# Kernel optimization log

Hardware: AMD Instinct MI355X
Metric: run time of the kernel (lower is better)

The kernel has to match this reference:

```python
import jax, jax.numpy as jnp
import numpy as np
import math

N_HEAD = 12
BLOCK = 256  # local attention block size (ls)
EPS = 1e-6


def _rotate(x):
    # pairs (a, b) -> (-b, a) over last dim (matches rotate_embeddings)
    a = x[..., 0::2]
    b = x[..., 1::2]
    return jnp.stack([-b, a], axis=-1).reshape(x.shape)


def setup_inputs() -> dict:
    key = jax.random.key(0)
    k1, k2, k3 = jax.random.split(key, 3)
    B, T, C = 4, 8192, 768
    s = 0.02
    return {
        "x": jax.random.normal(k1, (B, T, C), jnp.float32),
        "w_qkv": jax.random.normal(k2, (C, 3 * C), jnp.float32) * s,
        "w_ln": jnp.ones((C,), jnp.float32),
        "w_proj": jax.random.normal(k3, (C, C), jnp.float32) * s,
    }


def reference(x, w_qkv, w_ln, w_proj):
    B, T, C = x.shape
    nh, ls = N_HEAD, BLOCK
    hd = C // nh
    ng = T // ls

    xb = x.reshape(B, ng, ls, C)
    qkv = xb @ w_qkv                                   # (B,ng,ls,3C)
    q, k, v = jnp.split(qkv, 3, axis=-1)

    # QK RMSNorm over full embedding dim (before head split)
    def rms(t):
        return t * jax.lax.rsqrt(jnp.mean(t * t, axis=-1, keepdims=True) + EPS) * w_ln
    q, k = rms(q), rms(k)

    # split heads: (B,ng,nh,ls,hd)
    def heads(t):
        return jnp.swapaxes(t.reshape(B, ng, ls, nh, hd), 2, 3)
    q, k, v = heads(q), heads(k), heads(v)

    # RoPE (repo layout: freqs tiled via cat((ts,ts)), interleaved pair rotation)
    pos = 10000.0 ** ((-2.0 * jnp.arange(0, hd, 2, dtype=jnp.float32) - 1.0) / hd)
    ts = jnp.arange(ls, dtype=jnp.float32)[:, None] * pos[None, :]   # (ls, hd/2)
    rot = jnp.concatenate([ts, ts], axis=-1)                          # (ls, hd)
    cos, sin = jnp.cos(rot), jnp.sin(rot)
    q = q * cos + _rotate(q) * sin
    k = k * cos + _rotate(k) * sin

    # block-causal scores: causal only within each local block
    scale = 1.0 / math.sqrt(hd)
    att = jnp.einsum('bgnqd,bgnkd->bgnqk', q, k) * scale              # (B,ng,nh,ls,ls)
    mask = jnp.tril(jnp.ones((ls, ls), dtype=bool))
    att = jnp.where(mask, att, -jnp.finfo(att.dtype).max)
    att = jax.nn.softmax(att, axis=-1)
    y = jnp.einsum('bgnqk,bgnkd->bgnqd', att, v)                      # (B,ng,nh,ls,hd)

    y = jnp.swapaxes(y, 2, 3).reshape(B, ng, ls, C)
    y = y @ w_proj
    return y.reshape(B, T, C)
```

## Files before the change

### kernel.cpp

```cpp
#include <hip/hip_runtime.h>
#include <math.h>

typedef __attribute__((ext_vector_type(8))) short bf16x8;
typedef __attribute__((ext_vector_type(4))) short bf16x4;
typedef __attribute__((ext_vector_type(2))) short bf16x2;
typedef __attribute__((ext_vector_type(4))) float f32x4;

#define NH 12
#define HD 64
#define C0 768
#define C3 2304
#define LS 256

static __device__ __forceinline__ float bf2f(short u) {
  union { unsigned int i; float f; } c;
  c.i = ((unsigned int)(unsigned short)u) << 16;
  return c.f;
}
static __device__ __forceinline__ short f2bf(float f) {
  union { float f; unsigned int i; } c; c.f = f;
  unsigned int x = c.i;
  x += 0x7fffu + ((x >> 16) & 1u);
  return (short)(x >> 16);
}
static __device__ __forceinline__ unsigned pk2(float a, float b) {
  return (unsigned)(unsigned short)f2bf(a) | ((unsigned)(unsigned short)f2bf(b) << 16);
}

static __device__ __forceinline__ void gload_lds16(const short* g, const short* l) {
  unsigned long long ga = (unsigned long long)g;
  unsigned int la = (unsigned int)(unsigned long long)l;
  __builtin_amdgcn_global_load_lds(
      (const __attribute__((address_space(1))) void*)ga,
      (__attribute__((address_space(3))) void*)la, 16, 0, 0);
}

__global__ __launch_bounds__(256) void cast_kernel(const float* __restrict__ in,
                                                   short* __restrict__ out, int nquads) {
  int i = blockIdx.x * blockDim.x + threadIdx.x;
  int stride = gridDim.x * blockDim.x;
  for (; i < nquads; i += stride) {
    float4 v = ((const float4*)in)[i];
    bf16x4 o = { f2bf(v.x), f2bf(v.y), f2bf(v.z), f2bf(v.w) };
    ((bf16x4*)out)[i] = o;
  }
}

__global__ __launch_bounds__(256) void cast_transpose_kernel(const float* __restrict__ in,
                                                             short* __restrict__ out,
                                                             int K, int N) {
  __shared__ float tile[32][33];
  int n0 = blockIdx.x * 32, k0 = blockIdx.y * 32;
  int tx = threadIdx.x & 31, ty = threadIdx.x >> 5;
#pragma unroll
  for (int i = 0; i < 32; i += 8)
    tile[ty + i][tx] = in[(long)(k0 + ty + i) * N + n0 + tx];
  __syncthreads();
#pragma unroll
  for (int i = 0; i < 32; i += 8)
    out[(long)(n0 + ty + i) * K + k0 + tx] = f2bf(tile[tx][ty + i]);
}

__global__ void rope_tab_kernel(float* __restrict__ cost, float* __restrict__ sint) {
  int t = blockIdx.x, d = threadIdx.x;
  int i = d & 31;
  float freq = powf(10000.0f, -(float)(4 * i + 1) / 64.0f);
  float th = (float)t * freq;
  cost[t * 64 + d] = cosf(th);
  sint[t * 64 + d] = sinf(th);
}

#define PH_PRE                                         \
  __builtin_amdgcn_s_barrier();                        \
  __builtin_amdgcn_s_setprio(1);
#define PH_POST                                        \
  __builtin_amdgcn_s_setprio(0);                       \
  asm volatile("s_waitcnt lgkmcnt(0)" ::: "memory");   \
  __builtin_amdgcn_s_barrier();
#define PH_POSTV                                       \
  __builtin_amdgcn_s_setprio(0);                       \
  asm volatile("s_waitcnt lgkmcnt(0)" ::: "memory");   \
  asm volatile("s_waitcnt vmcnt(4)" ::: "memory");     \
  __builtin_amdgcn_s_barrier();
#define MMQ(MH, NP)                                                                \
  { _Pragma("unroll") for (int f_ = 0; f_ < 4; ++f_)                               \
      _Pragma("unroll") for (int n_ = 0; n_ < 2; ++n_)                             \
        _Pragma("unroll") for (int k_ = 0; k_ < 2; ++k_)                           \
          acc[(MH)*4 + f_][(NP)*2 + n_] = __builtin_amdgcn_mfma_f32_16x16x32_bf16( \
              af[f_*2 + k_], bfv[((NP)*2 + n_)*2 + k_],                            \
              acc[(MH)*4 + f_][(NP)*2 + n_], 0, 0, 0); }

template <int OUT_F32>
__global__ __launch_bounds__(512, 2) void gemm8p_kernel(const short* __restrict__ A,
                                                        const short* __restrict__ Bt,
                                                        void* __restrict__ Cout,
                                                        int N, int K, int nbn) {
  __shared__ short lds[65536];
  int t = threadIdx.x, lane = t & 63, wave = t >> 6;
  int lr = lane & 15, lg = lane >> 4;
  int wm = (wave >> 2) * 128, wn = (wave & 3) * 64;
  int id = blockIdx.x;
  int cpx = gridDim.x >> 3;
  int sw = (id & 7) * cpx + (id >> 3);
  int bm = sw / nbn, bn = sw % nbn;
  const short* Abase = A + (long)bm * 256 * K;
  const short* Bbase = Bt + (long)bn * 256 * K;
  int srow = t >> 3;
  int scol = ((t & 7) ^ (srow & 7)) * 8;
  int smax = K >> 4;

  f32x4 acc[8][4];
#pragma unroll
  for (int m = 0; m < 8; ++m)
#pragma unroll
    for (int n = 0; n < 4; ++n) acc[m][n] = (f32x4){0.f, 0.f, 0.f, 0.f};

  bf16x8 af[8], bfv[8];

  auto STAGE = [&](int s) {
    int slot = s & 3;
    int Tg = (s < smax) ? (s >> 2) : 0;
    const short* base = (slot & 2) ? Abase : Bbase;
    const short* g = base + (long)((slot & 1) * 128 + srow) * K + Tg * 64 + scol;
    int lb = ((s >> 2) & 1) * 32768 + ((slot >> 1) ^ 1) * 16384 + (slot & 1) * 8192 + t * 8;
    gload_lds16(g, &lds[lb]);
    gload_lds16(g + (long)64 * K, &lds[lb + 4096]);
  };
  auto LDA = [&](int b, int mh) {
#pragma unroll
    for (int f = 0; f < 4; ++f) {
      int R = wm + mh * 64 + f * 16 + lr;
      int rb = b * 32768 + R * 64;
      int s8 = R & 7;
      af[f * 2 + 0] = *(bf16x8*)&lds[rb + ((lg ^ s8) << 3)];
      af[f * 2 + 1] = *(bf16x8*)&lds[rb + (((4 + lg) ^ s8) << 3)];
    }
  };
  auto LDB = [&](int b, int nh) {
#pragma unroll
    for (int j = 0; j < 2; ++j) {
      int R = wn + (nh * 2 + j) * 16 + lr;
      int rb = b * 32768 + 16384 + R * 64;
      int s8 = R & 7;
      bfv[(nh * 2 + j) * 2 + 0] = *(bf16x8*)&lds[rb + ((lg ^ s8) << 3)];
      bfv[(nh * 2 + j) * 2 + 1] = *(bf16x8*)&lds[rb + (((4 + lg) ^ s8) << 3)];
    }
  };

  STAGE(0); STAGE(1); STAGE(2); STAGE(3); STAGE(4); STAGE(5);
  asm volatile("s_waitcnt vmcnt(4)" ::: "memory");
  __builtin_amdgcn_s_barrier();

  int iters = K >> 7;
  for (int i = 0; i < iters; ++i) {
    int si = 8 * i + 6;
    LDA(0, 0); LDB(0, 0);
    STAGE(si + 0);
    PH_PRE; MMQ(0, 0); PH_POST;
    LDB(0, 1);
    STAGE(si + 1);
    PH_PRE; MMQ(0, 1); PH_POST;
    LDA(0, 1);
    STAGE(si + 2);
    PH_PRE; MMQ(1, 0); PH_POST;
    STAGE(si + 3);
    PH_PRE; MMQ(1, 1); PH_POSTV;
    LDA(1, 0); LDB(1, 0);
    STAGE(si + 4);
    PH_PRE; MMQ(0, 0); PH_POST;
    LDB(1, 1);
    STAGE(si + 5);
    PH_PRE; MMQ(0, 1); PH_POST;
    LDA(1, 1);
    STAGE(si + 6);
    PH_PRE; MMQ(1, 0); PH_POST;
    STAGE(si + 7);
    PH_PRE; MMQ(1, 1); PH_POSTV;
  }

  long crow0 = (long)bm * 256 + wm;
  long ccol0 = (long)bn * 256 + wn;
#pragma unroll
  for (int f = 0; f < 8; ++f)
#pragma unroll
    for (int n = 0; n < 4; ++n)
#pragma unroll
      for (int r = 0; r < 4; ++r) {
        long row = crow0 + (f >> 2) * 64 + (f & 3) * 16 + lg * 4 + r;
        long col = ccol0 + n * 16 + lr;
        float v = acc[f][n][r];
        if (OUT_F32) ((float*)Cout)[row * N + col] = v;
        else ((short*)Cout)[row * N + col] = f2bf(v);
      }
}

__global__ __launch_bounds__(384) void norm_rope_kernel(short* __restrict__ QKV,
    const float* __restrict__ w_ln, const float* __restrict__ cost,
    const float* __restrict__ sint) {
  int row = blockIdx.x;
  int t = row & 255;
  int i = threadIdx.x;
  bool isq = i < 192;
  int e0 = (i - (isq ? 0 : 192)) * 4;
  long off = (long)row * C3 + (isq ? 0 : C0) + e0;
  bf16x4 v4 = *(const bf16x4*)&QKV[off];
  float a = bf2f(v4.x), b = bf2f(v4.y), c = bf2f(v4.z), d = bf2f(v4.w);
  float ss = a * a + b * b + c * c + d * d;
#pragma unroll
  for (int o = 32; o > 0; o >>= 1) ss += __shfl_down(ss, o);
  __shared__ float red[6];
  if ((i & 63) == 0) red[i >> 6] = ss;
  __syncthreads();
  float s3 = isq ? (red[0] + red[1] + red[2]) : (red[3] + red[4] + red[5]);
  float r = rsqrtf(s3 * (1.0f / 768.0f) + 1e-6f);
  float4 wl = *(const float4*)&w_ln[e0];
  int d0 = e0 & 63;
  float4 cs = *(const float4*)&cost[t * 64 + d0];
  float4 sn = *(const float4*)&sint[t * 64 + d0];
  float n0 = a * r * wl.x, n1 = b * r * wl.y, n2 = c * r * wl.z, n3 = d * r * wl.w;
  bf16x4 o;
  o.x = f2bf(n0 * cs.x - n1 * sn.x);
  o.y = f2bf(n1 * cs.y + n0 * sn.y);
  o.z = f2bf(n2 * cs.z - n3 * sn.z);
  o.w = f2bf(n3 * cs.w + n2 * sn.w);
  *(bf16x4*)&QKV[off] = o;
}

__global__ __launch_bounds__(512, 3) void attn_kernel(const short* __restrict__ QKV,
                                                      short* __restrict__ Y) {
  __shared__ short Ks[256 * 64];
  __shared__ short Vt[64 * 256];
  int blk = blockIdx.x;
  int bg = blk / NH, h = blk % NH;
  const long base = (long)bg * LS * C3 + h * HD;
  int tid = threadIdx.x, lane = tid & 63, wave = tid >> 6;
  int lr = lane & 15, lg = lane >> 4;

#pragma unroll
  for (int it = 0; it < 4; ++it) {
    int q = it * 512 + tid;
    int row = q >> 3, cp = q & 7;
    int gcp = cp ^ (row & 7);
    gload_lds16(QKV + base + (long)row * C3 + C0 + gcp * 8, &Ks[q * 8]);
  }
#pragma unroll
  for (int it = 0; it < 8; ++it) {
    int e = tid * 4 + it * 2048;
    int k = e >> 6, n = e & 63;
    bf16x4 v = *(const bf16x4*)&QKV[base + (long)k * C3 + 2 * C0 + n];
#pragma unroll
    for (int j = 0; j < 4; ++j) {
      int nn = n + j;
      Vt[nn * 256 + (((k >> 3) ^ (nn & 7)) << 3) + (k & 7)] = v[j];
    }
  }
  asm volatile("s_waitcnt vmcnt(0)" ::: "memory");
  __syncthreads();

  int addrA = (((lane >> 4) & 1) * 32 + lr) * 4;
  int addrB = addrA + 64;
  bool selhi = (lane & 32) != 0;

  for (int tt = 0; tt < 2; ++tt) {
    int tile = (tt == 0) ? wave : (15 - wave);
    int m0 = tile * 16;
    bf16x8 qf[2];
#pragma unroll
    for (int ks = 0; ks < 2; ++ks)
      qf[ks] = *(const bf16x8*)&QKV[base + (long)(m0 + lr) * C3 + ks * 32 + lg * 8];

    f32x4 zero4 = {0.f, 0.f, 0.f, 0.f};
    f32x4 accs[16];
#pragma unroll
    for (int n = 0; n < 16; ++n) accs[n] = zero4;

    __builtin_amdgcn_s_setprio(1);
#pragma unroll
    for (int n = 0; n < 16; ++n) {
      if (n <= tile) {
        int row = n * 16 + lr, sw = row & 7;
        bf16x8 k0 = *(bf16x8*)&Ks[row * 64 + ((lg ^ sw) << 3)];
        bf16x8 k1 = *(bf16x8*)&Ks[row * 64 + (((4 + lg) ^ sw) << 3)];
        accs[n] = __builtin_amdgcn_mfma_f32_16x16x32_bf16(k0, qf[0], accs[n], 0, 0, 0);
        accs[n] = __builtin_amdgcn_mfma_f32_16x16x32_bf16(k1, qf[1], accs[n], 0, 0, 0);
      }
    }
    __builtin_amdgcn_s_setprio(0);

    float tm[16];
#pragma unroll
    for (int n = 0; n < 16; ++n) {
      if (n <= tile) {
        if (n == tile) {
#pragma unroll
          for (int r = 0; r < 4; ++r)
            accs[n][r] = (lg * 4 + r <= lr) ? accs[n][r] : -1e30f;
        }
        float m01 = fmaxf(accs[n][0], accs[n][1]);
        float m23 = fmaxf(accs[n][2], accs[n][3]);
        tm[n] = fmaxf(m01, m23);
      } else {
        tm[n] = -1e30f;
      }
    }
#pragma unroll
    for (int st = 1; st < 16; st <<= 1)
#pragma unroll
      for (int j = 0; j < 16; j += 2 * st) tm[j] = fmaxf(tm[j], tm[j + st]);
    float mloc = tm[0];
    mloc = fmaxf(mloc, __shfl_xor(mloc, 16));
    mloc = fmaxf(mloc, __shfl_xor(mloc, 32));

    float ts[16];
#pragma unroll
    for (int n = 0; n < 16; ++n) {
      if (n <= tile) {
#pragma unroll
        for (int r = 0; r < 4; ++r) accs[n][r] = __expf((accs[n][r] - mloc) * 0.125f);
        float s01 = accs[n][0] + accs[n][1];
        float s23 = accs[n][2] + accs[n][3];
        ts[n] = s01 + s23;
      } else {
        ts[n] = 0.f;
      }
    }
#pragma unroll
    for (int st = 1; st < 16; st <<= 1)
#pragma unroll
      for (int j = 0; j < 16; j += 2 * st) ts[j] += ts[j + st];
    float s = ts[0];
    s += __shfl_xor(s, 16);
    s += __shfl_xor(s, 32);
    float rs = 1.0f / s;
    float rv[4];
#pragma unroll
    for (int r = 0; r < 4; ++r) {
      union { float f; int i; } c; c.f = rs;
      union { int i; float f; } o;
      o.i = __builtin_amdgcn_ds_bpermute((lg * 4 + r) * 4, c.i);
      rv[r] = o.f;
    }

    int ktmax = (m0 + 15) >> 5;
    f32x4 yacc[4];
#pragma unroll
    for (int n2 = 0; n2 < 4; ++n2) yacc[n2] = zero4;
#pragma unroll
    for (int kt = 0; kt < 8; ++kt) {
      if (kt <= ktmax) {
        int n0 = 2 * kt, n1 = 2 * kt + 1;
        unsigned a01_0 = pk2(accs[n0][0], accs[n0][1]);
        unsigned a23_0 = pk2(accs[n0][2], accs[n0][3]);
        unsigned a01_1 = (n1 <= tile) ? pk2(accs[n1][0], accs[n1][1]) : 0u;
        unsigned a23_1 = (n1 <= tile) ? pk2(accs[n1][2], accs[n1][3]) : 0u;
        union { unsigned u[4]; bf16x8 v; } af;
        unsigned g0a = (unsigned)__builtin_amdgcn_ds_bpermute(addrA, (int)a01_0);
        unsigned g0b = (unsigned)__builtin_amdgcn_ds_bpermute(addrA, (int)a01_1);
        unsigned g1a = (unsigned)__builtin_amdgcn_ds_bpermute(addrA, (int)a23_0);
        unsigned g1b = (unsigned)__builtin_amdgcn_ds_bpermute(addrA, (int)a23_1);
        unsigned g2a = (unsigned)__builtin_amdgcn_ds_bpermute(addrB, (int)a01_0);
        unsigned g2b = (unsigned)__builtin_amdgcn_ds_bpermute(addrB, (int)a01_1);
        unsigned g3a = (unsigned)__builtin_amdgcn_ds_bpermute(addrB, (int)a23_0);
        unsigned g3b = (unsigned)__builtin_amdgcn_ds_bpermute(addrB, (int)a23_1);
        af.u[0] = selhi ? g0b : g0a;
        af.u[1] = selhi ? g1b : g1a;
        af.u[2] = selhi ? g2b : g2a;
        af.u[3] = selhi ? g3b : g3a;
        int ac = kt * 32 + lg * 8;
        __builtin_amdgcn_s_setprio(1);
#pragma unroll
        for (int n2 = 0; n2 < 4; ++n2) {
          int vn = n2 * 16 + lr;
          bf16x8 vb = *(bf16x8*)&Vt[vn * 256 + (((ac >> 3) ^ (vn & 7)) << 3)];
          yacc[n2] = __builtin_amdgcn_mfma_f32_16x16x32_bf16(af.v, vb, yacc[n2], 0, 0, 0);
        }
        __builtin_amdgcn_s_setprio(0);
      }
    }

#pragma unroll
    for (int n2 = 0; n2 < 4; ++n2) {
#pragma unroll
      for (int r = 0; r < 4; ++r) {
        int row = m0 + lg * 4 + r, d = n2 * 16 + lr;
        Y[((long)(bg * LS + row)) * C0 + h * HD + d] = f2bf(yacc[n2][r] * rv[r]);
      }
    }
  }
}

extern "C" void kernel_launch(void* const* d_in, const int* in_sizes, int n_in,
                              void* d_out, int out_size, void* d_ws, size_t ws_size,
                              hipStream_t stream) {
  (void)in_sizes; (void)n_in; (void)out_size; (void)ws_size;
  const float* x = (const float*)d_in[0];
  const float* w_qkv = (const float*)d_in[1];
  const float* w_ln = (const float*)d_in[2];
  const float* w_proj = (const float*)d_in[3];
  float* out = (float*)d_out;

  char* ws = (char*)d_ws;
  short* Xb      = (short*)(ws + 0);
  short* QKV     = (short*)(ws + 50331648);
  short* Yb      = (short*)(ws + 201326592);
  short* WqkvT   = (short*)(ws + 251658240);
  short* WprojT  = (short*)(ws + 255197184);
  float* cost    = (float*)(ws + 256376832);
  float* sint    = (float*)(ws + 256442368);

  cast_kernel<<<2048, 256, 0, stream>>>(x, Xb, (4 * 8192 * C0) / 4);
  cast_transpose_kernel<<<dim3(C3 / 32, C0 / 32), 256, 0, stream>>>(w_qkv, WqkvT, C0, C3);
  cast_transpose_kernel<<<dim3(C0 / 32, C0 / 32), 256, 0, stream>>>(w_proj, WprojT, C0, C0);
  rope_tab_kernel<<<256, 64, 0, stream>>>(cost, sint);

  gemm8p_kernel<0><<<(C3 / 256) * (32768 / 256), 512, 0, stream>>>(Xb, WqkvT, QKV,
                                                                   C3, C0, C3 / 256);
  norm_rope_kernel<<<32768, 384, 0, stream>>>(QKV, w_ln, cost, sint);
  attn_kernel<<<128 * NH, 512, 0, stream>>>(QKV, Yb);
  gemm8p_kernel<1><<<(C0 / 256) * (32768 / 256), 512, 0, stream>>>(Yb, WprojT, out,
                                                                   C0, C0, C0 / 256);
}
```

Before: 326.8 us.

## Switch GEMMs to 32x32x16 MFMA with fragment-packed operands and a reworked pipeline

The cast kernels now write the inputs and weights into a pre-packed MFMA fragment layout, so the GEMM can load LDS fragments with simple contiguous lane reads. Both GEMMs move from 16x16x32 to 32x32x16 bf16 MFMA. The software pipeline is rescheduled so LDS reads and global-to-LDS stages run after the MFMA phase and are waited on with a vmcnt wait before each barrier. The projection GEMM keeps row-major A with XOR swizzle. The aim is fewer LDS instructions and better MFMA throughput, at the cost of a more complex packing step and correctness risk in the fragment mapping.

```diff
diff --git a/kernel.cpp b/kernel.cpp
--- a/kernel.cpp
+++ b/kernel.cpp
@@ -5,12 +5,14 @@
 typedef __attribute__((ext_vector_type(4))) short bf16x4;
 typedef __attribute__((ext_vector_type(2))) short bf16x2;
 typedef __attribute__((ext_vector_type(4))) float f32x4;
+typedef __attribute__((ext_vector_type(16))) float f32x16;
 
 #define NH 12
 #define HD 64
 #define C0 768
 #define C3 2304
 #define LS 256
+#define KT12 12
 
 static __device__ __forceinline__ float bf2f(short u) {
   union { unsigned int i; float f; } c;
@@ -35,30 +37,61 @@
       (__attribute__((address_space(3))) void*)la, 16, 0, 0);
 }
 
-__global__ __launch_bounds__(256) void cast_kernel(const float* __restrict__ in,
-                                                   short* __restrict__ out, int nquads) {
-  int i = blockIdx.x * blockDim.x + threadIdx.x;
-  int stride = gridDim.x * blockDim.x;
-  for (; i < nquads; i += stride) {
-    float4 v = ((const float4*)in)[i];
-    bf16x4 o = { f2bf(v.x), f2bf(v.y), f2bf(v.z), f2bf(v.w) };
-    ((bf16x4*)out)[i] = o;
-  }
-}
-
-__global__ __launch_bounds__(256) void cast_transpose_kernel(const float* __restrict__ in,
-                                                             short* __restrict__ out,
-                                                             int K, int N) {
-  __shared__ float tile[32][33];
-  int n0 = blockIdx.x * 32, k0 = blockIdx.y * 32;
-  int tx = threadIdx.x & 31, ty = threadIdx.x >> 5;
-#pragma unroll
-  for (int i = 0; i < 32; i += 8)
-    tile[ty + i][tx] = in[(long)(k0 + ty + i) * N + n0 + tx];
+__global__ __launch_bounds__(256) void cast_pack_A_kernel(const float* __restrict__ x,
+                                                          short* __restrict__ Apk) {
+  __shared__ short sb[256 * 64];
+  int bm = blockIdx.x, kt = blockIdx.y, t = threadIdx.x;
+#pragma unroll
+  for (int i = 0; i < 8; ++i) {
+    int seg = i * 256 + t;
+    int row = seg >> 3, sc = (seg & 7) * 8;
+    const float* src = x + ((long)(bm * 256 + row)) * C0 + kt * 64 + sc;
+    float4 v0 = *(const float4*)src;
+    float4 v1 = *(const float4*)(src + 4);
+    short* d = &sb[row * 64 + sc];
+    d[0] = f2bf(v0.x); d[1] = f2bf(v0.y); d[2] = f2bf(v0.z); d[3] = f2bf(v0.w);
+    d[4] = f2bf(v1.x); d[5] = f2bf(v1.y); d[6] = f2bf(v1.z); d[7] = f2bf(v1.w);
+  }
   __syncthreads();
 #pragma unroll
-  for (int i = 0; i < 32; i += 8)
-    out[(long)(n0 + ty + i) * K + k0 + tx] = f2bf(tile[tx][ty + i]);
+  for (int i = 0; i < 8; ++i) {
+    int c = i * 256 + t;
+    int l = c & 63, f = c >> 6;
+    int ks = f & 3, mt = (f >> 2) & 3, mh = f >> 4;
+    int row = mh * 128 + mt * 32 + (l & 31);
+    int kk = ks * 16 + (l >> 5) * 8;
+    bf16x8 v = *(bf16x8*)&sb[row * 64 + kk];
+    *(bf16x8*)&Apk[(((long)bm * KT12 + kt) * 2048 + c) * 8] = v;
+  }
+}
+
+__global__ __launch_bounds__(256) void cast_pack_B_kernel(const float* __restrict__ w,
+                                                          short* __restrict__ Bpk, int N) {
+  __shared__ short sb[256 * 64];
+  int bn = blockIdx.x, kt = blockIdx.y, t = threadIdx.x;
+#pragma unroll
+  for (int i = 0; i < 8; ++i) {
+    int seg = i * 256 + t;
+    int k = seg >> 5, nc = (seg & 31) * 8;
+    const float* src = w + ((long)(kt * 64 + k)) * N + bn * 256 + nc;
+    float4 v0 = *(const float4*)src;
+    float4 v1 = *(const float4*)(src + 4);
+    sb[(nc + 0) * 64 + k] = f2bf(v0.x); sb[(nc + 1) * 64 + k] = f2bf(v0.y);
+    sb[(nc + 2) * 64 + k] = f2bf(v0.z); sb[(nc + 3) * 64 + k] = f2bf(v0.w);
+    sb[(nc + 4) * 64 + k] = f2bf(v1.x); sb[(nc + 5) * 64 + k] = f2bf(v1.y);
+    sb[(nc + 6) * 64 + k] = f2bf(v1.z); sb[(nc + 7) * 64 + k] = f2bf(v1.w);
+  }
+  __syncthreads();
+#pragma unroll
+  for (int i = 0; i < 8; ++i) {
+    int c = i * 256 + t;
+    int l = c & 63, f = c >> 6;
+    int ks = f & 3, nt = (f >> 2) & 1, wng = f >> 3;
+    int col = wng * 64 + nt * 32 + (l & 31);
+    int kk = ks * 16 + (l >> 5) * 8;
+    bf16x8 v = *(bf16x8*)&sb[col * 64 + kk];
+    *(bf16x8*)&Bpk[(((long)bn * KT12 + kt) * 2048 + c) * 8] = v;
+  }
 }
 
 __global__ void rope_tab_kernel(float* __restrict__ cost, float* __restrict__ sint) {
@@ -70,125 +103,136 @@
   sint[t * 64 + d] = sinf(th);
 }
 
-#define PH_PRE                                         \
+#define PH_OPEN                                        \
   __builtin_amdgcn_s_barrier();                        \
+  asm volatile("s_waitcnt lgkmcnt(0)" ::: "memory");   \
+  __builtin_amdgcn_sched_barrier(0);                   \
   __builtin_amdgcn_s_setprio(1);
-#define PH_POST                                        \
-  __builtin_amdgcn_s_setprio(0);                       \
-  asm volatile("s_waitcnt lgkmcnt(0)" ::: "memory");   \
+#define PH_MID __builtin_amdgcn_s_setprio(0);
+#define PH_CLOSE                                       \
+  asm volatile("s_waitcnt vmcnt(2)" ::: "memory");     \
   __builtin_amdgcn_s_barrier();
-#define PH_POSTV                                       \
-  __builtin_amdgcn_s_setprio(0);                       \
-  asm volatile("s_waitcnt lgkmcnt(0)" ::: "memory");   \
-  asm volatile("s_waitcnt vmcnt(4)" ::: "memory");     \
-  __builtin_amdgcn_s_barrier();
-#define MMQ(MH, NP)                                                                \
-  { _Pragma("unroll") for (int f_ = 0; f_ < 4; ++f_)                               \
-      _Pragma("unroll") for (int n_ = 0; n_ < 2; ++n_)                             \
-        _Pragma("unroll") for (int k_ = 0; k_ < 2; ++k_)                           \
-          acc[(MH)*4 + f_][(NP)*2 + n_] = __builtin_amdgcn_mfma_f32_16x16x32_bf16( \
-              af[f_*2 + k_], bfv[((NP)*2 + n_)*2 + k_],                            \
-              acc[(MH)*4 + f_][(NP)*2 + n_], 0, 0, 0); }
-
-template <int OUT_F32>
-__global__ __launch_bounds__(512, 2) void gemm8p_kernel(const short* __restrict__ A,
-                                                        const short* __restrict__ Bt,
+#define MM8(ASET, BSET, MP, NT)                                                     \
+  { _Pragma("unroll") for (int m2_ = 0; m2_ < 2; ++m2_)                             \
+      _Pragma("unroll") for (int ks_ = 0; ks_ < 4; ++ks_)                           \
+        acc[(MP)*2 + m2_][NT] = __builtin_amdgcn_mfma_f32_32x32x16_bf16(            \
+            ASET[m2_ * 4 + ks_], BSET[ks_], acc[(MP)*2 + m2_][NT], 0, 0, 0); }
+
+template <int OUT_F32, int PACKED_A>
+__global__ __launch_bounds__(512, 2) void gemm32_kernel(const short* __restrict__ Apk,
+                                                        const short* __restrict__ Bpk,
+                                                        const short* __restrict__ Arm,
                                                         void* __restrict__ Cout,
                                                         int N, int K, int nbn) {
   __shared__ short lds[65536];
   int t = threadIdx.x, lane = t & 63, wave = t >> 6;
-  int lr = lane & 15, lg = lane >> 4;
-  int wm = (wave >> 2) * 128, wn = (wave & 3) * 64;
+  int wm = (wave >> 2) * 128, wng = wave & 3, wn = wng * 64, mh = wave >> 2;
   int id = blockIdx.x;
   int cpx = gridDim.x >> 3;
   int sw = (id & 7) * cpx + (id >> 3);
   int bm = sw / nbn, bn = sw % nbn;
-  const short* Abase = A + (long)bm * 256 * K;
-  const short* Bbase = Bt + (long)bn * 256 * K;
-  int srow = t >> 3;
-  int scol = ((t & 7) ^ (srow & 7)) * 8;
-  int smax = K >> 4;
-
-  f32x4 acc[8][4];
-#pragma unroll
-  for (int m = 0; m < 8; ++m)
-#pragma unroll
-    for (int n = 0; n < 4; ++n) acc[m][n] = (f32x4){0.f, 0.f, 0.f, 0.f};
-
-  bf16x8 af[8], bfv[8];
+
+  f32x16 acc[4][2];
+#pragma unroll
+  for (int m = 0; m < 4; ++m)
+#pragma unroll
+    for (int n = 0; n < 2; ++n)
+#pragma unroll
+      for (int r = 0; r < 16; ++r) acc[m][n][r] = 0.f;
+
+  bf16x8 a0[8], a1[8], b0[4], b1[4];
 
   auto STAGE = [&](int s) {
-    int slot = s & 3;
-    int Tg = (s < smax) ? (s >> 2) : 0;
-    const short* base = (slot & 2) ? Abase : Bbase;
-    const short* g = base + (long)((slot & 1) * 128 + srow) * K + Tg * 64 + scol;
-    int lb = ((s >> 2) & 1) * 32768 + ((slot >> 1) ^ 1) * 16384 + (slot & 1) * 8192 + t * 8;
-    gload_lds16(g, &lds[lb]);
-    gload_lds16(g + (long)64 * K, &lds[lb + 4096]);
+    if (s >= 4 * KT12) return;
+    int q = s & 3, Ts = s >> 2;
+    int bb = (Ts & 1) * 32768;
+    if (q < 2) {
+      if (PACKED_A) {
+        int c = q * 1024 + t;
+        const short* src = Apk + ((long)bm * KT12 + Ts) * 16384 + (long)c * 8;
+        gload_lds16(src, &lds[bb + c * 8]);
+        gload_lds16(src + 4096, &lds[bb + (c + 512) * 8]);
+      } else {
+        int row = q * 128 + (t >> 3);
+        int cr = q * 1024 + t;
+        const short* s1 = Arm + ((long)(bm * 256 + row)) * K + Ts * 64 + ((t & 7) ^ (row & 7)) * 8;
+        gload_lds16(s1, &lds[bb + cr * 8]);
+        int row2 = row + 64;
+        const short* s2 = Arm + ((long)(bm * 256 + row2)) * K + Ts * 64 + ((t & 7) ^ (row2 & 7)) * 8;
+        gload_lds16(s2, &lds[bb + (cr + 512) * 8]);
+      }
+    } else {
+      int c = (q - 2) * 1024 + t;
+      const short* src = Bpk + ((long)bn * KT12 + Ts) * 16384 + (long)c * 8;
+      gload_lds16(src, &lds[bb + 16384 + c * 8]);
+      gload_lds16(src + 4096, &lds[bb + 16384 + (c + 512) * 8]);
+    }
   };
-  auto LDA = [&](int b, int mh) {
-#pragma unroll
-    for (int f = 0; f < 4; ++f) {
-      int R = wm + mh * 64 + f * 16 + lr;
-      int rb = b * 32768 + R * 64;
-      int s8 = R & 7;
-      af[f * 2 + 0] = *(bf16x8*)&lds[rb + ((lg ^ s8) << 3)];
-      af[f * 2 + 1] = *(bf16x8*)&lds[rb + (((4 + lg) ^ s8) << 3)];
+  auto LDA = [&](bf16x8* d, int b, int mhalf) {
+    if (PACKED_A) {
+#pragma unroll
+      for (int m2 = 0; m2 < 2; ++m2)
+#pragma unroll
+        for (int ks = 0; ks < 4; ++ks)
+          d[m2 * 4 + ks] =
+              *(bf16x8*)&lds[b * 32768 + ((mh * 16 + (mhalf * 2 + m2) * 4 + ks) * 64 + lane) * 8];
+    } else {
+#pragma unroll
+      for (int m2 = 0; m2 < 2; ++m2)
+#pragma unroll
+        for (int ks = 0; ks < 4; ++ks) {
+          int row = wm + (mhalf * 2 + m2) * 32 + (lane & 31);
+          int g = (ks * 2 + (lane >> 5)) ^ (row & 7);
+          d[m2 * 4 + ks] = *(bf16x8*)&lds[b * 32768 + row * 64 + g * 8];
+        }
     }
   };
-  auto LDB = [&](int b, int nh) {
-#pragma unroll
-    for (int j = 0; j < 2; ++j) {
-      int R = wn + (nh * 2 + j) * 16 + lr;
-      int rb = b * 32768 + 16384 + R * 64;
-      int s8 = R & 7;
-      bfv[(nh * 2 + j) * 2 + 0] = *(bf16x8*)&lds[rb + ((lg ^ s8) << 3)];
-      bfv[(nh * 2 + j) * 2 + 1] = *(bf16x8*)&lds[rb + (((4 + lg) ^ s8) << 3)];
-    }
+  auto LDB = [&](bf16x8* d, int b, int nt) {
+#pragma unroll
+    for (int ks = 0; ks < 4; ++ks)
+      d[ks] = *(bf16x8*)&lds[b * 32768 + 16384 + ((wng * 8 + nt * 4 + ks) * 64 + lane) * 8];
   };
 
-  STAGE(0); STAGE(1); STAGE(2); STAGE(3); STAGE(4); STAGE(5);
-  asm volatile("s_waitcnt vmcnt(4)" ::: "memory");
+  for (int s = 0; s < 7; ++s) STAGE(s);
+  asm volatile("s_waitcnt vmcnt(6)" ::: "memory");
   __builtin_amdgcn_s_barrier();
-
-  int iters = K >> 7;
-  for (int i = 0; i < iters; ++i) {
-    int si = 8 * i + 6;
-    LDA(0, 0); LDB(0, 0);
-    STAGE(si + 0);
-    PH_PRE; MMQ(0, 0); PH_POST;
-    LDB(0, 1);
-    STAGE(si + 1);
-    PH_PRE; MMQ(0, 1); PH_POST;
-    LDA(0, 1);
-    STAGE(si + 2);
-    PH_PRE; MMQ(1, 0); PH_POST;
-    STAGE(si + 3);
-    PH_PRE; MMQ(1, 1); PH_POSTV;
-    LDA(1, 0); LDB(1, 0);
-    STAGE(si + 4);
-    PH_PRE; MMQ(0, 0); PH_POST;
-    LDB(1, 1);
-    STAGE(si + 5);
-    PH_PRE; MMQ(0, 1); PH_POST;
-    LDA(1, 1);
-    STAGE(si + 6);
-    PH_PRE; MMQ(1, 0); PH_POST;
-    STAGE(si + 7);
-    PH_PRE; MMQ(1, 1); PH_POSTV;
+  LDA(a0, 0, 0);
+  LDB(b0, 0, 0);
+  LDB(b1, 0, 1);
+
+  for (int it = 0; it < KT12 / 2; ++it) {
+    int P0 = 8 * it;
+    PH_OPEN; MM8(a0, b0, 0, 0); PH_MID;
+    LDA(a1, 0, 1); STAGE(P0 + 7); PH_CLOSE;
+    PH_OPEN; MM8(a0, b1, 0, 1); PH_MID;
+    LDA(a0, 1, 0); STAGE(P0 + 8); PH_CLOSE;
+    PH_OPEN; MM8(a1, b0, 1, 0); PH_MID;
+    LDB(b0, 1, 0); STAGE(P0 + 9); PH_CLOSE;
+    PH_OPEN; MM8(a1, b1, 1, 1); PH_MID;
+    LDB(b1, 1, 1); STAGE(P0 + 10); PH_CLOSE;
+    PH_OPEN; MM8(a0, b0, 0, 0); PH_MID;
+    LDA(a1, 1, 1); STAGE(P0 + 11); PH_CLOSE;
+    PH_OPEN; MM8(a0, b1, 0, 1); PH_MID;
+    LDA(a0, 0, 0); STAGE(P0 + 12); PH_CLOSE;
+    PH_OPEN; MM8(a1, b0, 1, 0); PH_MID;
+    LDB(b0, 0, 0); STAGE(P0 + 13); PH_CLOSE;
+    PH_OPEN; MM8(a1, b1, 1, 1); PH_MID;
+    LDB(b1, 0, 1); STAGE(P0 + 14); PH_CLOSE;
   }
 
   long crow0 = (long)bm * 256 + wm;
   long ccol0 = (long)bn * 256 + wn;
-#pragma unroll
-  for (int f = 0; f < 8; ++f)
-#pragma unroll
-    for (int n = 0; n < 4; ++n)
-#pragma unroll
-      for (int r = 0; r < 4; ++r) {
-        long row = crow0 + (f >> 2) * 64 + (f & 3) * 16 + lg * 4 + r;
-        long col = ccol0 + n * 16 + lr;
-        float v = acc[f][n][r];
+  int rbase = 4 * (lane >> 5);
+  int cl = lane & 31;
+#pragma unroll
+  for (int mt = 0; mt < 4; ++mt)
+#pragma unroll
+    for (int nt = 0; nt < 2; ++nt)
+#pragma unroll
+      for (int reg = 0; reg < 16; ++reg) {
+        long row = crow0 + mt * 32 + (reg & 3) + 8 * (reg >> 2) + rbase;
+        long col = ccol0 + nt * 32 + cl;
+        float v = acc[mt][nt][reg];
         if (OUT_F32) ((float*)Cout)[row * N + col] = v;
         else ((short*)Cout)[row * N + col] = f2bf(v);
       }
@@ -400,23 +444,23 @@
   float* out = (float*)d_out;
 
   char* ws = (char*)d_ws;
-  short* Xb      = (short*)(ws + 0);
+  short* Apk     = (short*)(ws + 0);
   short* QKV     = (short*)(ws + 50331648);
   short* Yb      = (short*)(ws + 201326592);
-  short* WqkvT   = (short*)(ws + 251658240);
-  short* WprojT  = (short*)(ws + 255197184);
+  short* WqkvPk  = (short*)(ws + 251658240);
+  short* WprojPk = (short*)(ws + 255197184);
   float* cost    = (float*)(ws + 256376832);
   float* sint    = (float*)(ws + 256442368);
 
-  cast_kernel<<<2048, 256, 0, stream>>>(x, Xb, (4 * 8192 * C0) / 4);
-  cast_transpose_kernel<<<dim3(C3 / 32, C0 / 32), 256, 0, stream>>>(w_qkv, WqkvT, C0, C3);
-  cast_transpose_kernel<<<dim3(C0 / 32, C0 / 32), 256, 0, stream>>>(w_proj, WprojT, C0, C0);
+  cast_pack_A_kernel<<<dim3(128, KT12), 256, 0, stream>>>(x, Apk);
+  cast_pack_B_kernel<<<dim3(9, KT12), 256, 0, stream>>>(w_qkv, WqkvPk, C3);
+  cast_pack_B_kernel<<<dim3(3, KT12), 256, 0, stream>>>(w_proj, WprojPk, C0);
   rope_tab_kernel<<<256, 64, 0, stream>>>(cost, sint);
 
-  gemm8p_kernel<0><<<(C3 / 256) * (32768 / 256), 512, 0, stream>>>(Xb, WqkvT, QKV,
-                                                                   C3, C0, C3 / 256);
+  gemm32_kernel<0, 1><<<128 * 9, 512, 0, stream>>>(Apk, WqkvPk, nullptr, QKV,
+                                                   C3, C0, 9);
   norm_rope_kernel<<<32768, 384, 0, stream>>>(QKV, w_ln, cost, sint);
   attn_kernel<<<128 * NH, 512, 0, stream>>>(QKV, Yb);
-  gemm8p_kernel<1><<<(C0 / 256) * (32768 / 256), 512, 0, stream>>>(Yb, WprojT, out,
-                                                                   C0, C0, C0 / 256);
-}
+  gemm32_kernel<1, 0><<<128 * 3, 512, 0, stream>>>(nullptr, WprojPk, Yb, out,
+                                                   C0, C0, 3);
+}
```

New measurement: 373.0 us. 1.14x slower.

## Use 128x128 prepacked-B GEMM for projection and wave-per-row norm/rope

Applied to the files above, without the earlier changes.

Replaces the 256x256-tile GEMM for the output projection with a new 128x128-tile kernel that uses 32x32x16 MFMAs and a pre-packed B operand laid out in fragment order, so it can be loaded with contiguous direct-to-LDS loads. The smaller tile raises the block count from 384 to 1536 for better CU occupancy on the N=768 GEMM. The norm/rope kernel is also restructured to one wave per q or k row, with shuffle-only reduction and wider loads, which removes the LDS reduction and the block barrier. A new cast-and-pack kernel prepares w_proj in that layout. The trade-offs are less data reuse per tile and a simpler double-buffered pipeline with a full wait on every K step.

```diff
diff --git a/kernel.cpp b/kernel.cpp
--- a/kernel.cpp
+++ b/kernel.cpp
@@ -5,12 +5,14 @@
 typedef __attribute__((ext_vector_type(4))) short bf16x4;
 typedef __attribute__((ext_vector_type(2))) short bf16x2;
 typedef __attribute__((ext_vector_type(4))) float f32x4;
+typedef __attribute__((ext_vector_type(16))) float f32x16;
 
 #define NH 12
 #define HD 64
 #define C0 768
 #define C3 2304
 #define LS 256
+#define KT12 12
 
 static __device__ __forceinline__ float bf2f(short u) {
   union { unsigned int i; float f; } c;
@@ -59,6 +61,37 @@
 #pragma unroll
   for (int i = 0; i < 32; i += 8)
     out[(long)(n0 + ty + i) * K + k0 + tx] = f2bf(tile[tx][ty + i]);
+}
+
+template <int WNG>
+__global__ __launch_bounds__(256) void cast_pack_B_kernel(const float* __restrict__ w,
+                                                          short* __restrict__ Bpk, int N) {
+  __shared__ short sb[WNG * 64 * 64];
+  int bn = blockIdx.x, kt = blockIdx.y, t = threadIdx.x;
+#pragma unroll
+  for (int i = 0; i < WNG * 2; ++i) {
+    int seg = i * 256 + t;
+    int k = seg / (WNG * 8);
+    int nc = (seg % (WNG * 8)) * 8;
+    const float* src = w + ((long)(kt * 64 + k)) * N + bn * (WNG * 64) + nc;
+    float4 v0 = *(const float4*)src;
+    float4 v1 = *(const float4*)(src + 4);
+    sb[(nc + 0) * 64 + k] = f2bf(v0.x); sb[(nc + 1) * 64 + k] = f2bf(v0.y);
+    sb[(nc + 2) * 64 + k] = f2bf(v0.z); sb[(nc + 3) * 64 + k] = f2bf(v0.w);
+    sb[(nc + 4) * 64 + k] = f2bf(v1.x); sb[(nc + 5) * 64 + k] = f2bf(v1.y);
+    sb[(nc + 6) * 64 + k] = f2bf(v1.z); sb[(nc + 7) * 64 + k] = f2bf(v1.w);
+  }
+  __syncthreads();
+#pragma unroll
+  for (int i = 0; i < WNG * 2; ++i) {
+    int c = i * 256 + t;
+    int l = c & 63, f = c >> 6;
+    int ks = f & 3, nt = (f >> 2) & 1, wng = f >> 3;
+    int col = wng * 64 + nt * 32 + (l & 31);
+    int kk = ks * 16 + (l >> 5) * 8;
+    bf16x8 v = *(bf16x8*)&sb[col * 64 + kk];
+    *(bf16x8*)&Bpk[(((long)bn * KT12 + kt) * (WNG * 512) + c) * 8] = v;
+  }
 }
 
 __global__ void rope_tab_kernel(float* __restrict__ cost, float* __restrict__ sint) {
@@ -194,36 +227,151 @@
       }
 }
 
-__global__ __launch_bounds__(384) void norm_rope_kernel(short* __restrict__ QKV,
+template <int OUT_F32>
+__global__ __launch_bounds__(256, 2) void gemm128_kernel(const short* __restrict__ Arm,
+                                                         const short* __restrict__ Bpk,
+                                                         void* __restrict__ Cout,
+                                                         int N, int K, int nbn) {
+  __shared__ short lds[32768];
+  int t = threadIdx.x, lane = t & 63, wave = t >> 6;
+  int wm = (wave >> 1) * 64, wng = wave & 1;
+  int id = blockIdx.x;
+  int cpx = gridDim.x >> 3;
+  int sw = (id & 7) * cpx + (id >> 3);
+  int bm = sw / nbn, bn = sw % nbn;
+  int l31 = lane & 31, lh = lane >> 5;
+
+  f32x16 acc[2][2];
+#pragma unroll
+  for (int m = 0; m < 2; ++m)
+#pragma unroll
+    for (int n = 0; n < 2; ++n)
+#pragma unroll
+      for (int r = 0; r < 16; ++r) acc[m][n][r] = 0.f;
+
+  auto STAGE = [&](int T) {
+    int bb = (T & 1) * 16384;
+#pragma unroll
+    for (int i = 0; i < 4; ++i) {
+      int q = i * 256 + t;
+      int row = q >> 3, cp = q & 7;
+      const short* ga = Arm + ((long)(bm * 128 + row)) * K + T * 64 + ((cp ^ (row & 7)) * 8);
+      gload_lds16(ga, &lds[bb + q * 8]);
+      const short* gb = Bpk + ((long)bn * KT12 + T) * 8192 + (long)q * 8;
+      gload_lds16(gb, &lds[bb + 8192 + q * 8]);
+    }
+  };
+
+  STAGE(0);
+  asm volatile("s_waitcnt vmcnt(0)" ::: "memory");
+  __builtin_amdgcn_s_barrier();
+
+  for (int T = 0; T < KT12; ++T) {
+    int bb = (T & 1) * 16384;
+    if (T + 1 < KT12) STAGE(T + 1);
+    bf16x8 a[2][4], b[2][4];
+#pragma unroll
+    for (int mt = 0; mt < 2; ++mt) {
+      int row = wm + mt * 32 + l31;
+      int s8 = row & 7;
+#pragma unroll
+      for (int ks = 0; ks < 4; ++ks) {
+        int g = (ks * 2 + lh) ^ s8;
+        a[mt][ks] = *(bf16x8*)&lds[bb + row * 64 + g * 8];
+      }
+    }
+#pragma unroll
+    for (int nt = 0; nt < 2; ++nt)
+#pragma unroll
+      for (int ks = 0; ks < 4; ++ks)
+        b[nt][ks] = *(bf16x8*)&lds[bb + 8192 + (((wng * 2 + nt) * 4 + ks) * 64 + lane) * 8];
+    __builtin_amdgcn_s_setprio(1);
+#pragma unroll
+    for (int mt = 0; mt < 2; ++mt)
+#pragma unroll
+      for (int nt = 0; nt < 2; ++nt)
+#pragma unroll
+        for (int ks = 0; ks < 4; ++ks)
+          acc[mt][nt] = __builtin_amdgcn_mfma_f32_32x32x16_bf16(a[mt][ks], b[nt][ks],
+                                                                acc[mt][nt], 0, 0, 0);
+    __builtin_amdgcn_s_setprio(0);
+    asm volatile("s_waitcnt lgkmcnt(0)" ::: "memory");
+    asm volatile("s_waitcnt vmcnt(0)" ::: "memory");
+    __builtin_amdgcn_s_barrier();
+  }
+
+  long crow0 = (long)bm * 128 + wm;
+  long ccol0 = (long)bn * 128 + wng * 64;
+  int rbase = 4 * lh;
+#pragma unroll
+  for (int mt = 0; mt < 2; ++mt)
+#pragma unroll
+    for (int nt = 0; nt < 2; ++nt)
+#pragma unroll
+      for (int reg = 0; reg < 16; ++reg) {
+        long row = crow0 + mt * 32 + (reg & 3) + 8 * (reg >> 2) + rbase;
+        long col = ccol0 + nt * 32 + l31;
+        float v = acc[mt][nt][reg];
+        if (OUT_F32) ((float*)Cout)[row * N + col] = v;
+        else ((short*)Cout)[row * N + col] = f2bf(v);
+      }
+}
+
+__global__ __launch_bounds__(512) void norm_rope_kernel(short* __restrict__ QKV,
     const float* __restrict__ w_ln, const float* __restrict__ cost,
     const float* __restrict__ sint) {
-  int row = blockIdx.x;
+  int wid = (blockIdx.x << 3) + (threadIdx.x >> 6);
+  int lane = threadIdx.x & 63;
+  int row = wid >> 1;
   int t = row & 255;
-  int i = threadIdx.x;
-  bool isq = i < 192;
-  int e0 = (i - (isq ? 0 : 192)) * 4;
-  long off = (long)row * C3 + (isq ? 0 : C0) + e0;
-  bf16x4 v4 = *(const bf16x4*)&QKV[off];
-  float a = bf2f(v4.x), b = bf2f(v4.y), c = bf2f(v4.z), d = bf2f(v4.w);
-  float ss = a * a + b * b + c * c + d * d;
-#pragma unroll
-  for (int o = 32; o > 0; o >>= 1) ss += __shfl_down(ss, o);
-  __shared__ float red[6];
-  if ((i & 63) == 0) red[i >> 6] = ss;
-  __syncthreads();
-  float s3 = isq ? (red[0] + red[1] + red[2]) : (red[3] + red[4] + red[5]);
-  float r = rsqrtf(s3 * (1.0f / 768.0f) + 1e-6f);
-  float4 wl = *(const float4*)&w_ln[e0];
-  int d0 = e0 & 63;
-  float4 cs = *(const float4*)&cost[t * 64 + d0];
-  float4 sn = *(const float4*)&sint[t * 64 + d0];
-  float n0 = a * r * wl.x, n1 = b * r * wl.y, n2 = c * r * wl.z, n3 = d * r * wl.w;
-  bf16x4 o;
-  o.x = f2bf(n0 * cs.x - n1 * sn.x);
-  o.y = f2bf(n1 * cs.y + n0 * sn.y);
-  o.z = f2bf(n2 * cs.z - n3 * sn.z);
-  o.w = f2bf(n3 * cs.w + n2 * sn.w);
-  *(bf16x4*)&QKV[off] = o;
+  long base = (long)row * C3 + (wid & 1) * C0;
+  int e8 = lane * 8, e4 = 512 + lane * 4;
+  bf16x8 v8 = *(const bf16x8*)&QKV[base + e8];
+  bf16x4 v4 = *(const bf16x4*)&QKV[base + e4];
+  float f[12];
+#pragma unroll
+  for (int j = 0; j < 8; ++j) f[j] = bf2f(v8[j]);
+#pragma unroll
+  for (int j = 0; j < 4; ++j) f[8 + j] = bf2f(v4[j]);
+  float ss = 0.f;
+#pragma unroll
+  for (int j = 0; j < 12; ++j) ss += f[j] * f[j];
+#pragma unroll
+  for (int o = 32; o > 0; o >>= 1) ss += __shfl_xor(ss, o);
+  float r = rsqrtf(ss * (1.0f / 768.0f) + 1e-6f);
+  float4 w0 = *(const float4*)&w_ln[e8];
+  float4 w1 = *(const float4*)&w_ln[e8 + 4];
+  float4 w2 = *(const float4*)&w_ln[e4];
+  float n[12];
+  n[0] = f[0] * r * w0.x;  n[1] = f[1] * r * w0.y;
+  n[2] = f[2] * r * w0.z;  n[3] = f[3] * r * w0.w;
+  n[4] = f[4] * r * w1.x;  n[5] = f[5] * r * w1.y;
+  n[6] = f[6] * r * w1.z;  n[7] = f[7] * r * w1.w;
+  n[8] = f[8] * r * w2.x;  n[9] = f[9] * r * w2.y;
+  n[10] = f[10] * r * w2.z; n[11] = f[11] * r * w2.w;
+  int d8 = e8 & 63, d4 = e4 & 63;
+  const float* cb = cost + t * 64;
+  const float* sbp = sint + t * 64;
+  float4 c0 = *(const float4*)&cb[d8], c1 = *(const float4*)&cb[d8 + 4];
+  float4 c2 = *(const float4*)&cb[d4];
+  float4 s0 = *(const float4*)&sbp[d8], s1 = *(const float4*)&sbp[d8 + 4];
+  float4 s2 = *(const float4*)&sbp[d4];
+  bf16x8 o8;
+  bf16x4 o4;
+  o8[0] = f2bf(n[0] * c0.x - n[1] * s0.x);
+  o8[1] = f2bf(n[1] * c0.y + n[0] * s0.y);
+  o8[2] = f2bf(n[2] * c0.z - n[3] * s0.z);
+  o8[3] = f2bf(n[3] * c0.w + n[2] * s0.w);
+  o8[4] = f2bf(n[4] * c1.x - n[5] * s1.x);
+  o8[5] = f2bf(n[5] * c1.y + n[4] * s1.y);
+  o8[6] = f2bf(n[6] * c1.z - n[7] * s1.z);
+  o8[7] = f2bf(n[7] * c1.w + n[6] * s1.w);
+  o4[0] = f2bf(n[8] * c2.x - n[9] * s2.x);
+  o4[1] = f2bf(n[9] * c2.y + n[8] * s2.y);
+  o4[2] = f2bf(n[10] * c2.z - n[11] * s2.z);
+  o4[3] = f2bf(n[11] * c2.w + n[10] * s2.w);
+  *(bf16x8*)&QKV[base + e8] = o8;
+  *(bf16x4*)&QKV[base + e4] = o4;
 }
 
 __global__ __launch_bounds__(512, 3) void attn_kernel(const short* __restrict__ QKV,
@@ -404,19 +552,18 @@
   short* QKV     = (short*)(ws + 50331648);
   short* Yb      = (short*)(ws + 201326592);
   short* WqkvT   = (short*)(ws + 251658240);
-  short* WprojT  = (short*)(ws + 255197184);
+  short* WprojPk = (short*)(ws + 255197184);
   float* cost    = (float*)(ws + 256376832);
   float* sint    = (float*)(ws + 256442368);
 
   cast_kernel<<<2048, 256, 0, stream>>>(x, Xb, (4 * 8192 * C0) / 4);
   cast_transpose_kernel<<<dim3(C3 / 32, C0 / 32), 256, 0, stream>>>(w_qkv, WqkvT, C0, C3);
-  cast_transpose_kernel<<<dim3(C0 / 32, C0 / 32), 256, 0, stream>>>(w_proj, WprojT, C0, C0);
+  cast_pack_B_kernel<2><<<dim3(6, KT12), 256, 0, stream>>>(w_proj, WprojPk, C0);
   rope_tab_kernel<<<256, 64, 0, stream>>>(cost, sint);
 
   gemm8p_kernel<0><<<(C3 / 256) * (32768 / 256), 512, 0, stream>>>(Xb, WqkvT, QKV,
                                                                    C3, C0, C3 / 256);
-  norm_rope_kernel<<<32768, 384, 0, stream>>>(QKV, w_ln, cost, sint);
+  norm_rope_kernel<<<8192, 512, 0, stream>>>(QKV, w_ln, cost, sint);
   attn_kernel<<<128 * NH, 512, 0, stream>>>(QKV, Yb);
-  gemm8p_kernel<1><<<(C0 / 256) * (32768 / 256), 512, 0, stream>>>(Yb, WprojT, out,
-                                                                   C0, C0, C0 / 256);
-}
+  gemm128_kernel<1><<<256 * 6, 256, 0, stream>>>(Yb, WprojPk, out, C0, C0, 6);
+}
```

After: 316.3 us. -3.2%, faster.
